# Optimization experiments

Measured on AMD Instinct MI355X. Metric: run time of the kernel, lower is better.

The kernel has to match this reference:

```python
import jax, jax.numpy as jnp
import numpy as np

SEQ_LEN, BATCH, INPUT_SIZE, HIDDEN = 512, 256, 64, 256


def setup_inputs() -> dict:
    key = jax.random.key(0)
    kx, kwx, kbx, kwh, kbh = jax.random.split(key, 5)
    s_in = 1.0 / np.sqrt(INPUT_SIZE)
    s_h = 1.0 / np.sqrt(HIDDEN)
    return {
        "x": jax.random.normal(kx, (SEQ_LEN, BATCH, INPUT_SIZE), dtype=jnp.float32),
        # nn.Linear params: weight [out, in], bias [out]
        "Wx": jax.random.uniform(kwx, (HIDDEN, INPUT_SIZE), jnp.float32, -s_in, s_in),
        "bx": jax.random.uniform(kbx, (HIDDEN,), jnp.float32, -s_in, s_in),
        "Wh": jax.random.uniform(kwh, (HIDDEN, HIDDEN), jnp.float32, -s_h, s_h),
        "bh": jax.random.uniform(kbh, (HIDDEN,), jnp.float32, -s_h, s_h),
    }


def reference(x, Wx, bx, Wh, bh):
    # Precompute the input projection for all timesteps as one batched GEMM.
    # xp: (seq_len, batch, hidden)
    xp = jnp.einsum("sbi,hi->sbh", x, Wx) + bx
    h0 = jnp.zeros((x.shape[1], Wh.shape[0]), dtype=x.dtype)

    def step(h, xp_t):
        h_new = jnp.tanh(h @ Wh.T + bh + xp_t)
        return h_new, h_new

    h_last, h_seq = jax.lax.scan(step, h0, xp)
    return h_seq, h_last[None]  # (seq, batch, hidden), (1, batch, hidden)
```

## Files before the change

kernel.cpp:

```cpp
#include <hip/hip_runtime.h>
#include <cmath>

#define S 512
#define B 256
#define IN 64
#define H 256
#define HPAD 20

typedef float v2f __attribute__((ext_vector_type(2)));
typedef float v4f __attribute__((ext_vector_type(4)));


template<int CTRL>
__device__ __forceinline__ float dpp_mov(float v) {
    return __int_as_float(__builtin_amdgcn_update_dpp(
        0, __float_as_int(v), CTRL, 0xF, 0xF, true));
}

template<int CTRL>
__device__ __forceinline__ float comb(bool hi, float a, float b) {
    const float u = hi ? b : a;
    const float w = hi ? a : b;
    return u + dpp_mov<CTRL>(w);
}

#define PK_MUL(d, a, b) \
    asm("v_pk_mul_f32 %0, %1, %2" : "=v"(d) : "v"(a), "v"(b))
#define PK_FMA(d, a, b) \
    asm("v_pk_fma_f32 %0, %1, %2, %0" : "+v"(d) : "v"(a), "v"(b))

__global__ __launch_bounds__(512, 2) void rnn_fused5(
    const float* __restrict__ x,
    const float* __restrict__ Wx,
    const float* __restrict__ bx,
    const float* __restrict__ Wh,
    const float* __restrict__ bh,
    float* __restrict__ out)
{
    __shared__ __align__(16) float h_buf[2][16 * HPAD];
    __shared__ __align__(16) float x_buf[2][IN];

    const int tid = threadIdx.x;
    const int s   = tid & 15;
    const int jg  = tid >> 4;
    const int b   = blockIdx.x;

    v2f wh2[8][8];
    v2f wx2[8][2];
    #pragma unroll
    for (int r = 0; r < 8; ++r) {
        const int j = 8 * jg + r;
        const v4f* whp = (const v4f*)(Wh + (size_t)j * H + 16 * s);
        #pragma unroll
        for (int q = 0; q < 4; ++q) {
            const v4f t = whp[q];
            wh2[r][2 * q]     = t.lo;
            wh2[r][2 * q + 1] = t.hi;
        }
        const v4f tx = *(const v4f*)(Wx + (size_t)j * IN + 4 * s);
        wx2[r][0] = tx.lo;
        wx2[r][1] = tx.hi;
    }
    #pragma unroll
    for (int r = 0; r < 8; ++r)
        asm volatile("" : "+v"(wh2[r][0]), "+v"(wh2[r][1]), "+v"(wh2[r][2]),
                          "+v"(wh2[r][3]), "+v"(wh2[r][4]), "+v"(wh2[r][5]),
                          "+v"(wh2[r][6]), "+v"(wh2[r][7]),
                          "+v"(wx2[r][0]), "+v"(wx2[r][1]));

    const int jown = 8 * jg + (s & 7);
    const float bias = bh[jown] + bx[jown];
    const bool b0 = (s & 1) != 0;
    const bool b1 = (s & 2) != 0;
    const bool b2 = (s & 4) != 0;

    if (tid < 16 * HPAD) h_buf[0][tid] = 0.f;
    const v4f* xsrc = (const v4f*)(x + (size_t)b * IN) + tid;
    if (tid < 16) {
        ((v4f*)x_buf[0])[tid] = *xsrc;
        xsrc += (B * IN) / 4;
    }

    const int jw    = 8 * jg + s;
    const int hwoff = (jw >> 4) * HPAD + (jw & 15);
    float* outp = out + (size_t)b * H + jw;
    float last_h = 0.f;

    __syncthreads();

    int p = 0;
    for (int t = 0; t < S; ++t) {
        const v4f xv = ((const v4f*)x_buf[p])[s];
        const v2f xlo = xv.lo, xhi = xv.hi;
        const v4f* hb = (const v4f*)(h_buf[p] + HPAD * s);
        v2f hh[8];
        #pragma unroll
        for (int q = 0; q < 4; ++q) {
            const v4f hq = hb[q];
            hh[2 * q]     = hq.lo;
            hh[2 * q + 1] = hq.hi;
        }

        v4f xn;
        const bool pf = (tid < 16) && (t < S - 1);
        if (pf) { xn = *xsrc; xsrc += (B * IN) / 4; }

        v2f acc2[8];
        #pragma unroll
        for (int r = 0; r < 8; ++r) PK_MUL(acc2[r], wx2[r][0], xlo);
        #pragma unroll
        for (int r = 0; r < 8; ++r) PK_FMA(acc2[r], wx2[r][1], xhi);
        #pragma unroll
        for (int k = 0; k < 8; ++k) {
            #pragma unroll
            for (int r = 0; r < 8; ++r) PK_FMA(acc2[r], wh2[r][k], hh[k]);
        }

        float acc[8];
        #pragma unroll
        for (int r = 0; r < 8; ++r) acc[r] = acc2[r].x + acc2[r].y;
        #pragma unroll
        for (int r = 0; r < 8; ++r) acc[r] += dpp_mov<0x140>(acc[r]);
        #pragma unroll
        for (int r = 0; r < 8; ++r) acc[r] += dpp_mov<0x141>(acc[r]);
        const float n0 = comb<0x4E>(b1, acc[0], acc[2]);
        const float n1 = comb<0x4E>(b1, acc[1], acc[3]);
        const float n4 = comb<0x4E>(b1, acc[4], acc[6]);
        const float n5 = comb<0x4E>(b1, acc[5], acc[7]);
        const float m0 = comb<0xB1>(b0, n0, n1);
        const float m4 = comb<0xB1>(b0, n4, n5);
        const float total = b2 ? m4 : m0;

        if (s < 8) {
            const float sum = total + bias;
            const float pre = fminf(fmaxf(sum, -15.f), 15.f);
            const float e   = __expf(2.f * pre);
            const float hv  = (e - 1.f) * __builtin_amdgcn_rcpf(e + 1.f);
            last_h = hv;
            h_buf[p ^ 1][hwoff] = hv;
            *outp = hv;
            outp += B * H;
        }
        if (pf) ((v4f*)x_buf[p ^ 1])[tid] = xn;

        __syncthreads();
        p ^= 1;
    }

    if (s < 8)
        out[(size_t)S * B * H + (size_t)b * H + jw] = last_h;
}

extern "C" void kernel_launch(void* const* d_in, const int* in_sizes, int n_in,
                              void* d_out, int out_size, void* d_ws, size_t ws_size,
                              hipStream_t stream) {
    const float* x  = (const float*)d_in[0];
    const float* Wx = (const float*)d_in[1];
    const float* bx = (const float*)d_in[2];
    const float* Wh = (const float*)d_in[3];
    const float* bh = (const float*)d_in[4];
    float* out = (float*)d_out;

    rnn_fused5<<<dim3(B), dim3(512), 0, stream>>>(x, Wx, bx, Wh, bh, out);
}
```

Before: 488.2 us.

## Split hidden units across 1024 threads with four rows per thread group

```diff
diff --git a/kernel.cpp b/kernel.cpp
--- a/kernel.cpp
+++ b/kernel.cpp
@@ -29,7 +29,7 @@
 #define PK_FMA(d, a, b) \
     asm("v_pk_fma_f32 %0, %1, %2, %0" : "+v"(d) : "v"(a), "v"(b))
 
-__global__ __launch_bounds__(512, 2) void rnn_fused5(
+__global__ __launch_bounds__(1024, 4) void rnn_fused7(
     const float* __restrict__ x,
     const float* __restrict__ Wx,
     const float* __restrict__ bx,
@@ -45,11 +45,11 @@
     const int jg  = tid >> 4;
     const int b   = blockIdx.x;
 
-    v2f wh2[8][8];
-    v2f wx2[8][2];
+    v2f wh2[4][8];
+    v2f wx2[4][2];
     #pragma unroll
-    for (int r = 0; r < 8; ++r) {
-        const int j = 8 * jg + r;
+    for (int r = 0; r < 4; ++r) {
+        const int j = 4 * jg + r;
         const v4f* whp = (const v4f*)(Wh + (size_t)j * H + 16 * s);
         #pragma unroll
         for (int q = 0; q < 4; ++q) {
@@ -62,17 +62,16 @@
         wx2[r][1] = tx.hi;
     }
     #pragma unroll
-    for (int r = 0; r < 8; ++r)
+    for (int r = 0; r < 4; ++r)
         asm volatile("" : "+v"(wh2[r][0]), "+v"(wh2[r][1]), "+v"(wh2[r][2]),
                           "+v"(wh2[r][3]), "+v"(wh2[r][4]), "+v"(wh2[r][5]),
                           "+v"(wh2[r][6]), "+v"(wh2[r][7]),
                           "+v"(wx2[r][0]), "+v"(wx2[r][1]));
 
-    const int jown = 8 * jg + (s & 7);
+    const int jown = 4 * jg + (s & 3);
     const float bias = bh[jown] + bx[jown];
     const bool b0 = (s & 1) != 0;
     const bool b1 = (s & 2) != 0;
-    const bool b2 = (s & 4) != 0;
 
     if (tid < 16 * HPAD) h_buf[0][tid] = 0.f;
     const v4f* xsrc = (const v4f*)(x + (size_t)b * IN) + tid;
@@ -81,73 +80,67 @@
         xsrc += (B * IN) / 4;
     }
 
-    const int jw    = 8 * jg + s;
+    const int jw    = 4 * jg + s;
     const int hwoff = (jw >> 4) * HPAD + (jw & 15);
     float* outp = out + (size_t)b * H + jw;
     float last_h = 0.f;
 
     __syncthreads();
 
-    int p = 0;
-    for (int t = 0; t < S; ++t) {
-        const v4f xv = ((const v4f*)x_buf[p])[s];
-        const v2f xlo = xv.lo, xhi = xv.hi;
-        const v4f* hb = (const v4f*)(h_buf[p] + HPAD * s);
-        v2f hh[8];
-        #pragma unroll
-        for (int q = 0; q < 4; ++q) {
-            const v4f hq = hb[q];
-            hh[2 * q]     = hq.lo;
-            hh[2 * q + 1] = hq.hi;
-        }
-
-        v4f xn;
-        const bool pf = (tid < 16) && (t < S - 1);
-        if (pf) { xn = *xsrc; xsrc += (B * IN) / 4; }
-
-        v2f acc2[8];
-        #pragma unroll
-        for (int r = 0; r < 8; ++r) PK_MUL(acc2[r], wx2[r][0], xlo);
-        #pragma unroll
-        for (int r = 0; r < 8; ++r) PK_FMA(acc2[r], wx2[r][1], xhi);
-        #pragma unroll
-        for (int k = 0; k < 8; ++k) {
-            #pragma unroll
-            for (int r = 0; r < 8; ++r) PK_FMA(acc2[r], wh2[r][k], hh[k]);
-        }
-
-        float acc[8];
-        #pragma unroll
-        for (int r = 0; r < 8; ++r) acc[r] = acc2[r].x + acc2[r].y;
-        #pragma unroll
-        for (int r = 0; r < 8; ++r) acc[r] += dpp_mov<0x140>(acc[r]);
-        #pragma unroll
-        for (int r = 0; r < 8; ++r) acc[r] += dpp_mov<0x141>(acc[r]);
-        const float n0 = comb<0x4E>(b1, acc[0], acc[2]);
-        const float n1 = comb<0x4E>(b1, acc[1], acc[3]);
-        const float n4 = comb<0x4E>(b1, acc[4], acc[6]);
-        const float n5 = comb<0x4E>(b1, acc[5], acc[7]);
-        const float m0 = comb<0xB1>(b0, n0, n1);
-        const float m4 = comb<0xB1>(b0, n4, n5);
-        const float total = b2 ? m4 : m0;
-
-        if (s < 8) {
-            const float sum = total + bias;
-            const float pre = fminf(fmaxf(sum, -15.f), 15.f);
-            const float e   = __expf(2.f * pre);
-            const float hv  = (e - 1.f) * __builtin_amdgcn_rcpf(e + 1.f);
-            last_h = hv;
-            h_buf[p ^ 1][hwoff] = hv;
-            *outp = hv;
-            outp += B * H;
-        }
-        if (pf) ((v4f*)x_buf[p ^ 1])[tid] = xn;
-
-        __syncthreads();
-        p ^= 1;
+#define STEP(CUR, NXT, TT)                                                    \
+    {                                                                         \
+        const v4f xv = ((const v4f*)x_buf[CUR])[s];                           \
+        const v4f* hbp = (const v4f*)(h_buf[CUR] + HPAD * s);                 \
+        const v4f q0 = hbp[0], q1 = hbp[1], q2 = hbp[2], q3 = hbp[3];         \
+        v2f hh[8];                                                            \
+        hh[0] = q0.lo; hh[1] = q0.hi; hh[2] = q1.lo; hh[3] = q1.hi;           \
+        hh[4] = q2.lo; hh[5] = q2.hi; hh[6] = q3.lo; hh[7] = q3.hi;           \
+        v4f xn;                                                               \
+        const bool pf = (tid < 16) && ((TT) < S - 1);                         \
+        if (pf) { xn = *xsrc; xsrc += (B * IN) / 4; }                         \
+        v2f acc2[4];                                                          \
+        _Pragma("unroll")                                                     \
+        for (int r = 0; r < 4; ++r) PK_MUL(acc2[r], wx2[r][0], xv.lo);        \
+        _Pragma("unroll")                                                     \
+        for (int r = 0; r < 4; ++r) PK_FMA(acc2[r], wx2[r][1], xv.hi);        \
+        _Pragma("unroll")                                                     \
+        for (int k = 0; k < 8; ++k) {                                         \
+            _Pragma("unroll")                                                 \
+            for (int r = 0; r < 4; ++r) PK_FMA(acc2[r], wh2[r][k], hh[k]);    \
+        }                                                                     \
+        float c[4];                                                           \
+        _Pragma("unroll")                                                     \
+        for (int r = 0; r < 4; ++r) c[r] = acc2[r].x + acc2[r].y;             \
+          \
+        _Pragma("unroll")                                                     \
+        for (int r = 0; r < 4; ++r) c[r] += dpp_mov<0x141>(c[r]);             \
+        _Pragma("unroll")                                                     \
+        for (int r = 0; r < 4; ++r) c[r] += dpp_mov<0x140>(c[r]);             \
+                    \
+        const float n0 = comb<0x4E>(b1, c[0], c[2]);                          \
+        const float n1 = comb<0x4E>(b1, c[1], c[3]);                          \
+        const float m  = comb<0xB1>(b0, n0, n1);      \
+        if (s < 4) {                                                          \
+            const float sum = m + bias;                                       \
+            const float pre = fminf(fmaxf(sum, -15.f), 15.f);                 \
+            const float e   = __builtin_amdgcn_exp2f(pre * 2.88539008177793f);\
+            const float hv  = (e - 1.f) * __builtin_amdgcn_rcpf(e + 1.f);     \
+            last_h = hv;                                                      \
+            h_buf[NXT][hwoff] = hv;                                           \
+            *outp = hv;                   \
+            outp += B * H;                                                    \
+        }                                                                     \
+        if (pf) ((v4f*)x_buf[NXT])[tid] = xn;                                 \
+        __syncthreads();                                                      \
     }
 
-    if (s < 8)
+    for (int t2 = 0; t2 < S / 2; ++t2) {
+        STEP(0, 1, 2 * t2);
+        STEP(1, 0, 2 * t2 + 1);
+    }
+#undef STEP
+
+    if (s < 4)
         out[(size_t)S * B * H + (size_t)b * H + jw] = last_h;
 }
 
@@ -161,5 +154,5 @@
     const float* bh = (const float*)d_in[4];
     float* out = (float*)d_out;
 
-    rnn_fused5<<<dim3(B), dim3(512), 0, stream>>>(x, Wx, bx, Wh, bh, out);
+    rnn_fused7<<<dim3(B), dim3(1024), 0, stream>>>(x, Wx, bx, Wh, bh, out);
 }
```

New measurement: 473.6 us. 3.0% less time.
